# Kernel tuning notes

Hardware: AMD Instinct MI355X
Metric: run time of the kernel (lower is better)

The kernel has to match this reference:

```python
import jax, jax.numpy as jnp
import numpy as np

N_NODES = 100_000
N_EDGES = 1_600_000
N_FEAT = 128
N_HID = 64
N_CLASS = 10
N_LAYERS = 3
N_GRAPHS = 1000


def _linear_init(key, fan_in, fan_out):
    kw, kb = jax.random.split(key)
    s = 1.0 / np.sqrt(fan_in)
    w = jax.random.uniform(kw, (fan_in, fan_out), minval=-s, maxval=s, dtype=jnp.float32)
    b = jax.random.uniform(kb, (fan_out,), minval=-s, maxval=s, dtype=jnp.float32)
    return w, b


def setup_inputs() -> dict:
    key = jax.random.key(0)
    ks = jax.random.split(key, 16)
    x = jax.random.normal(ks[0], (N_NODES, N_FEAT), dtype=jnp.float32)
    edge_index = jax.random.randint(ks[1], (2, N_EDGES), 0, N_NODES, dtype=jnp.int64)
    batch = jnp.sort(jax.random.randint(ks[2], (N_NODES,), 0, N_GRAPHS, dtype=jnp.int64))

    pre_w, pre_b = _linear_init(ks[3], N_FEAT, N_HID)
    w1s, b1s, w2s, b2s = [], [], [], []
    for l in range(N_LAYERS):
        w1, b1 = _linear_init(jax.random.fold_in(ks[4], 2 * l), N_HID, N_HID)
        w2, b2 = _linear_init(jax.random.fold_in(ks[4], 2 * l + 1), N_HID, N_HID)
        w1s.append(w1); b1s.append(b1); w2s.append(w2); b2s.append(b2)
    post_w, post_b = _linear_init(ks[5], N_HID, N_HID)
    ro_w, ro_b = _linear_init(ks[6], N_HID, N_CLASS)

    return {
        "x": x, "edge_index": edge_index, "batch": batch,
        "pre_w": pre_w, "pre_b": pre_b,
        "conv_w1": jnp.stack(w1s), "conv_b1": jnp.stack(b1s),
        "conv_w2": jnp.stack(w2s), "conv_b2": jnp.stack(b2s),
        "post_w": post_w, "post_b": post_b,
        "ro_w": ro_w, "ro_b": ro_b,
    }


def reference(x, edge_index, batch, pre_w, pre_b, conv_w1, conv_b1, conv_w2, conv_b2, post_w, post_b, ro_w, ro_b):
    src = edge_index[0]  # message source (x_j)
    dst = edge_index[1]  # message target

    h = x @ pre_w + pre_b  # [N, H]
    for l in range(N_LAYERS):
        # GINConv, eps=0: MLP((1+eps)*h_i + sum_{j in N(i)} h_j)
        agg = jax.ops.segment_sum(h[src], dst, num_segments=N_NODES)
        z = h + agg
        z = jax.nn.relu(z @ conv_w1[l] + conv_b1[l]) @ conv_w2[l] + conv_b2[l]
        h = jax.nn.relu(z)  # dropout is identity in eval mode

    g = jax.ops.segment_sum(h, batch, num_segments=N_GRAPHS)  # global_add_pool [G, H]
    g = jax.nn.relu(g @ post_w + post_b)
    logits = g @ ro_w + ro_b
    return jax.nn.log_softmax(logits, axis=1)
```

## Files before the change

kernel.cpp:

```cpp
#include <hip/hip_runtime.h>
#include <math.h>

#define N_NODES  100000
#define N_FEAT   128
#define N_HID    64
#define N_CLASS  10
#define N_GRAPHS 1000
#define N_EDGES  1600000
#define NTILES   1563
#define BLK_N    128
#define NT2      782
#define HF_GROUPS 8
#define HF_RANGE 12500
#define HF_BLOCKS 2048
#define CSR_STRIDE 64
#define EMAX_LDS 32

typedef int iv4 __attribute__((ext_vector_type(4)));

__device__ __forceinline__ float bflo(unsigned u) { return __uint_as_float(u << 16); }
__device__ __forceinline__ float bfhi(unsigned u) { return __uint_as_float(u & 0xffff0000u); }
__device__ __forceinline__ unsigned bf_rne(float f) {
    unsigned u = __float_as_uint(f);
    return (u + 0x7fffu + ((u >> 16) & 1u)) >> 16;
}
__device__ __forceinline__ unsigned pack2(float a, float b) {
    return bf_rne(a) | (bf_rne(b) << 16);
}

__global__ __launch_bounds__(256, 4) void pre_kernel(
    const float* __restrict__ x, const float* __restrict__ W,
    const float* __restrict__ b, uint2* __restrict__ h)
{
    __shared__ float xs[64][68];
    __shared__ float ws[64][68];
    const int tid = threadIdx.x;
    const int tx = tid & 15, ty = tid >> 4;
    const int n0 = blockIdx.x * 64;

    float acc[4][4];
#pragma unroll
    for (int i = 0; i < 4; ++i)
#pragma unroll
        for (int j = 0; j < 4; ++j) acc[i][j] = 0.f;

    for (int p = 0; p < 2; ++p) {
        __syncthreads();
#pragma unroll
        for (int t = 0; t < 4; ++t) {
            const int idx = t * 256 + tid;
            const int m = idx >> 4, kv = idx & 15;
            float4 v = make_float4(0.f, 0.f, 0.f, 0.f);
            if (n0 + m < N_NODES)
                v = *(const float4*)(x + (size_t)(n0 + m) * N_FEAT + p * 64 + kv * 4);
            *(float4*)&xs[m][kv * 4] = v;
            *(float4*)&ws[m][kv * 4] =
                *(const float4*)(W + (size_t)(p * 64 + m) * N_HID + kv * 4);
        }
        __syncthreads();
#pragma unroll 2
        for (int k4 = 0; k4 < 16; ++k4) {
            float4 a[4], bb[4];
#pragma unroll
            for (int i = 0; i < 4; ++i)
                a[i] = *(const float4*)&xs[ty + 16 * i][k4 * 4];
#pragma unroll
            for (int j = 0; j < 4; ++j)
                bb[j] = *(const float4*)&ws[k4 * 4 + j][tx * 4];
#pragma unroll
            for (int i = 0; i < 4; ++i) {
                const float* ap = (const float*)&a[i];
#pragma unroll
                for (int j = 0; j < 4; ++j) {
                    const float* bp = (const float*)&bb[j];
#pragma unroll
                    for (int c = 0; c < 4; ++c)
                        acc[i][c] = fmaf(ap[j], bp[c], acc[i][c]);
                }
            }
        }
    }

    const float4 bias = *(const float4*)(b + tx * 4);
#pragma unroll
    for (int i = 0; i < 4; ++i) {
        const int node = n0 + ty + 16 * i;
        if (node < N_NODES) {
            h[(size_t)node * 16 + tx] = make_uint2(
                pack2(acc[i][0] + bias.x, acc[i][1] + bias.y),
                pack2(acc[i][2] + bias.z, acc[i][3] + bias.w));
        }
    }
}

__global__ __launch_bounds__(256) void hist_fill_kernel(
    const int* __restrict__ ei, int* __restrict__ deg, int* __restrict__ csr)
{
    const int r   = blockIdx.x & (HF_GROUPS - 1);
    const int g   = blockIdx.x >> 3;
    const int lo  = r * HF_RANGE;
    const int hi  = lo + HF_RANGE;
    const int gsz = (gridDim.x >> 3) * blockDim.x;
    const int t0  = g * blockDim.x + threadIdx.x;
    const iv4* dst4 = (const iv4*)(ei + N_EDGES);
    for (int q = t0; q < N_EDGES / 4; q += gsz) {
        const iv4 d = __builtin_nontemporal_load(dst4 + q);
        const int e0 = q * 4;
        if (d.x >= lo && d.x < hi) {
            int p = atomicAdd(&deg[d.x], 1);
            if (p < CSR_STRIDE)
                csr[d.x * CSR_STRIDE + p] = __builtin_nontemporal_load(ei + e0);
        }
        if (d.y >= lo && d.y < hi) {
            int p = atomicAdd(&deg[d.y], 1);
            if (p < CSR_STRIDE)
                csr[d.y * CSR_STRIDE + p] = __builtin_nontemporal_load(ei + e0 + 1);
        }
        if (d.z >= lo && d.z < hi) {
            int p = atomicAdd(&deg[d.z], 1);
            if (p < CSR_STRIDE)
                csr[d.z * CSR_STRIDE + p] = __builtin_nontemporal_load(ei + e0 + 2);
        }
        if (d.w >= lo && d.w < hi) {
            int p = atomicAdd(&deg[d.w], 1);
            if (p < CSR_STRIDE)
                csr[d.w * CSR_STRIDE + p] = __builtin_nontemporal_load(ei + e0 + 3);
        }
    }
}

__global__ __launch_bounds__(512, 6) void gather_mlp_kernel(
    const uint2* __restrict__ hin, uint2* __restrict__ hout,
    const int* __restrict__ csr, const int* __restrict__ deg,
    const float* __restrict__ W1, const float* __restrict__ b1,
    const float* __restrict__ W2, const float* __restrict__ b2)
{
    __shared__ float as[BLK_N][68];
    __shared__ float ws[64][68];
    __shared__ int   sdeg[BLK_N];
    const int tid = threadIdx.x;
    const int tx = tid & 15, ty = tid >> 4;
    const int sub = tx;
    const int n0 = blockIdx.x * BLK_N;

#pragma unroll
    for (int t = 0; t < 2; ++t) {
        const int idx = t * 512 + tid;
        const int m = idx >> 4, kv = idx & 15;
        *(float4*)&ws[m][kv * 4] = *(const float4*)(W1 + (size_t)m * N_HID + kv * 4);
    }
    if (tid < BLK_N) {
        const int node = n0 + tid;
        sdeg[tid] = (node < N_NODES) ? deg[node] : 0;
    }
#pragma unroll
    for (int t = 0; t < 2; ++t) {
        const int idx = t * 512 + tid;
        const int r = idx >> 3, s4 = idx & 7;
        const int node = n0 + r;
        int4 v = make_int4(0, 0, 0, 0);
        if (node < N_NODES)
            v = *(const int4*)(csr + (size_t)node * CSR_STRIDE + s4 * 4);
        *(int4*)((int*)&as[r][36] + s4 * 4) = v;
    }
    __syncthreads();

    for (int pp = 0; pp < 2; ++pp) {
        const int rA = ty + 64 * pp;
        const int rB = rA + 32;
        const int nodeA = n0 + rA;
        const int nodeB = n0 + rB;
        float aAx = 0.f, aAy = 0.f, aAz = 0.f, aAw = 0.f;
        float bAx = 0.f, bAy = 0.f, bAz = 0.f, bAw = 0.f;
        float aBx = 0.f, aBy = 0.f, aBz = 0.f, aBw = 0.f;
        float bBx = 0.f, bBy = 0.f, bBz = 0.f, bBw = 0.f;
        int nA = 0, nB = 0;
        if (nodeA < N_NODES) {
            nA = sdeg[rA]; nA = nA > CSR_STRIDE ? CSR_STRIDE : nA;
            const uint2 s = hin[(size_t)nodeA * 16 + sub];
            aAx = bflo(s.x); aAy = bfhi(s.x); aAz = bflo(s.y); aAw = bfhi(s.y);
        }
        if (nodeB < N_NODES) {
            nB = sdeg[rB]; nB = nB > CSR_STRIDE ? CSR_STRIDE : nB;
            const uint2 s = hin[(size_t)nodeB * 16 + sub];
            aBx = bflo(s.x); aBy = bfhi(s.x); aBz = bflo(s.y); aBw = bfhi(s.y);
        }
        const int nnA = nA > EMAX_LDS ? EMAX_LDS : nA;
        const int nnB = nB > EMAX_LDS ? EMAX_LDS : nB;
        const int* epA = (const int*)&as[rA][36];
        const int* epB = (const int*)&as[rB][36];
        const int mx = nnA > nnB ? nnA : nnB;
        for (int eb = 0; eb < mx; eb += 8) {
            uint2 rvA[8], rvB[8];
            const bool doA = eb < nnA;
            const bool doB = eb < nnB;
            if (doA) {
#pragma unroll
                for (int u = 0; u < 8; ++u) {
                    const int idx = eb + u;
                    const int cl = idx < nnA ? idx : nnA - 1;
                    rvA[u] = hin[(size_t)epA[cl] * 16 + sub];
                }
            }
            if (doB) {
#pragma unroll
                for (int u = 0; u < 8; ++u) {
                    const int idx = eb + u;
                    const int cl = idx < nnB ? idx : nnB - 1;
                    rvB[u] = hin[(size_t)epB[cl] * 16 + sub];
                }
            }
            if (doA) {
#pragma unroll
                for (int u = 0; u < 8; u += 2) {
                    if (eb + u < nnA) {
                        aAx += bflo(rvA[u].x); aAy += bfhi(rvA[u].x);
                        aAz += bflo(rvA[u].y); aAw += bfhi(rvA[u].y);
                    }
                    if (eb + u + 1 < nnA) {
                        bAx += bflo(rvA[u + 1].x); bAy += bfhi(rvA[u + 1].x);
                        bAz += bflo(rvA[u + 1].y); bAw += bfhi(rvA[u + 1].y);
                    }
                }
            }
            if (doB) {
#pragma unroll
                for (int u = 0; u < 8; u += 2) {
                    if (eb + u < nnB) {
                        aBx += bflo(rvB[u].x); aBy += bfhi(rvB[u].x);
                        aBz += bflo(rvB[u].y); aBw += bfhi(rvB[u].y);
                    }
                    if (eb + u + 1 < nnB) {
                        bBx += bflo(rvB[u + 1].x); bBy += bfhi(rvB[u + 1].x);
                        bBz += bflo(rvB[u + 1].y); bBw += bfhi(rvB[u + 1].y);
                    }
                }
            }
        }
        for (int t = EMAX_LDS; t < nA; ++t) {
            const int s0 = csr[(size_t)nodeA * CSR_STRIDE + t];
            const uint2 a = hin[(size_t)s0 * 16 + sub];
            aAx += bflo(a.x); aAy += bfhi(a.x);
            aAz += bflo(a.y); aAw += bfhi(a.y);
        }
        for (int t = EMAX_LDS; t < nB; ++t) {
            const int s0 = csr[(size_t)nodeB * CSR_STRIDE + t];
            const uint2 a = hin[(size_t)s0 * 16 + sub];
            aBx += bflo(a.x); aBy += bfhi(a.x);
            aBz += bflo(a.y); aBw += bfhi(a.y);
        }
        *(float4*)&as[rA][sub * 4] =
            make_float4(aAx + bAx, aAy + bAy, aAz + bAz, aAw + bAw);
        *(float4*)&as[rB][sub * 4] =
            make_float4(aBx + bBx, aBy + bBy, aBz + bBz, aBw + bBw);
    }
    __syncthreads();

    float acc[4][4];
#pragma unroll
    for (int i = 0; i < 4; ++i)
#pragma unroll
        for (int j = 0; j < 4; ++j) acc[i][j] = 0.f;
#pragma unroll 2
    for (int k4 = 0; k4 < 16; ++k4) {
        float4 a[4], bb[4];
#pragma unroll
        for (int i = 0; i < 4; ++i)
            a[i] = *(const float4*)&as[ty + 32 * i][k4 * 4];
#pragma unroll
        for (int j = 0; j < 4; ++j)
            bb[j] = *(const float4*)&ws[k4 * 4 + j][tx * 4];
#pragma unroll
        for (int i = 0; i < 4; ++i) {
            const float* ap = (const float*)&a[i];
#pragma unroll
            for (int j = 0; j < 4; ++j) {
                const float* bp = (const float*)&bb[j];
#pragma unroll
                for (int c = 0; c < 4; ++c)
                    acc[i][c] = fmaf(ap[j], bp[c], acc[i][c]);
            }
        }
    }
    const float4 bias1 = *(const float4*)(b1 + tx * 4);
    float4 z[4];
#pragma unroll
    for (int i = 0; i < 4; ++i) {
        z[i].x = fmaxf(acc[i][0] + bias1.x, 0.f);
        z[i].y = fmaxf(acc[i][1] + bias1.y, 0.f);
        z[i].z = fmaxf(acc[i][2] + bias1.z, 0.f);
        z[i].w = fmaxf(acc[i][3] + bias1.w, 0.f);
    }
    __syncthreads();
#pragma unroll
    for (int i = 0; i < 4; ++i)
        *(float4*)&as[ty + 32 * i][tx * 4] = z[i];
#pragma unroll
    for (int t = 0; t < 2; ++t) {
        const int idx = t * 512 + tid;
        const int m = idx >> 4, kv = idx & 15;
        *(float4*)&ws[m][kv * 4] = *(const float4*)(W2 + (size_t)m * N_HID + kv * 4);
    }
    __syncthreads();

#pragma unroll
    for (int i = 0; i < 4; ++i)
#pragma unroll
        for (int j = 0; j < 4; ++j) acc[i][j] = 0.f;
#pragma unroll 2
    for (int k4 = 0; k4 < 16; ++k4) {
        float4 a[4], bb[4];
#pragma unroll
        for (int i = 0; i < 4; ++i)
            a[i] = *(const float4*)&as[ty + 32 * i][k4 * 4];
#pragma unroll
        for (int j = 0; j < 4; ++j)
            bb[j] = *(const float4*)&ws[k4 * 4 + j][tx * 4];
#pragma unroll
        for (int i = 0; i < 4; ++i) {
            const float* ap = (const float*)&a[i];
#pragma unroll
            for (int j = 0; j < 4; ++j) {
                const float* bp = (const float*)&bb[j];
#pragma unroll
                for (int c = 0; c < 4; ++c)
                    acc[i][c] = fmaf(ap[j], bp[c], acc[i][c]);
            }
        }
    }
    const float4 bias2 = *(const float4*)(b2 + tx * 4);
#pragma unroll
    for (int i = 0; i < 4; ++i) {
        const int node = n0 + ty + 32 * i;
        if (node < N_NODES) {
            hout[(size_t)node * 16 + tx] = make_uint2(
                pack2(fmaxf(acc[i][0] + bias2.x, 0.f),
                      fmaxf(acc[i][1] + bias2.y, 0.f)),
                pack2(fmaxf(acc[i][2] + bias2.z, 0.f),
                      fmaxf(acc[i][3] + bias2.w, 0.f)));
        }
    }
}

__global__ __launch_bounds__(256) void pool_head_kernel(
    const unsigned short* __restrict__ h, const int* __restrict__ batch,
    const float* __restrict__ Wp, const float* __restrict__ bp,
    const float* __restrict__ Wr, const float* __restrict__ br,
    float* __restrict__ out)
{
    const int graph = blockIdx.x;
    int l = 0, r = N_NODES;
    while (l < r) { int m = (l + r) >> 1; if (batch[m] < graph) l = m + 1; else r = m; }
    const int lo = l;
    r = N_NODES;
    while (l < r) { int m = (l + r) >> 1; if (batch[m] < graph + 1) l = m + 1; else r = m; }
    const int hi = l;

    const int lane = threadIdx.x & 63;
    const int wave = threadIdx.x >> 6;
    float acc = 0.0f;
    for (int i = lo + wave; i < hi; i += 4)
        acc += __uint_as_float(((unsigned)h[(size_t)i * N_HID + lane]) << 16);
    __shared__ float sacc[4][N_HID];
    sacc[wave][lane] = acc;
    __syncthreads();
    if (wave != 0) return;

    const float gv = sacc[0][lane] + sacc[1][lane] + sacc[2][lane] + sacc[3][lane];
    float acc2 = bp[lane];
#pragma unroll
    for (int k = 0; k < N_HID; ++k) {
        const float gk = __int_as_float(
            __builtin_amdgcn_readlane(__float_as_int(gv), k));
        acc2 = fmaf(gk, Wp[k * N_HID + lane], acc2);
    }
    const float y = fmaxf(acc2, 0.f);

    float logit = (lane < N_CLASS) ? br[lane] : 0.f;
#pragma unroll
    for (int k = 0; k < N_HID; ++k) {
        const float yk = __int_as_float(
            __builtin_amdgcn_readlane(__float_as_int(y), k));
        if (lane < N_CLASS)
            logit = fmaf(yk, Wr[k * N_CLASS + lane], logit);
    }

    __shared__ float slog[N_CLASS];
    if (lane < N_CLASS) slog[lane] = logit;
    if (lane < N_CLASS) {
        float m = -INFINITY;
#pragma unroll
        for (int c = 0; c < N_CLASS; ++c) m = fmaxf(m, slog[c]);
        float sum = 0.0f;
#pragma unroll
        for (int c = 0; c < N_CLASS; ++c) sum += expf(slog[c] - m);
        out[(size_t)graph * N_CLASS + lane] = logit - m - logf(sum);
    }
}

extern "C" void kernel_launch(void* const* d_in, const int* in_sizes, int n_in,
                              void* d_out, int out_size, void* d_ws, size_t ws_size,
                              hipStream_t stream)
{
    const float* x       = (const float*)d_in[0];
    const int*   ei      = (const int*)d_in[1];
    const int*   batch   = (const int*)d_in[2];
    const float* pre_w   = (const float*)d_in[3];
    const float* pre_b   = (const float*)d_in[4];
    const float* conv_w1 = (const float*)d_in[5];
    const float* conv_b1 = (const float*)d_in[6];
    const float* conv_w2 = (const float*)d_in[7];
    const float* conv_b2 = (const float*)d_in[8];
    const float* post_w  = (const float*)d_in[9];
    const float* post_b  = (const float*)d_in[10];
    const float* ro_w    = (const float*)d_in[11];
    const float* ro_b    = (const float*)d_in[12];
    float* out = (float*)d_out;

    uint2* h0   = (uint2*)d_ws;
    uint2* h1   = h0 + (size_t)N_NODES * 16;
    int*   deg  = (int*)(h1 + (size_t)N_NODES * 16);
    int*   csr  = deg + N_NODES;

    (void)hipMemsetAsync(deg, 0, N_NODES * sizeof(int), stream);

    pre_kernel<<<NTILES, 256, 0, stream>>>(x, pre_w, pre_b, h0);
    hist_fill_kernel<<<HF_BLOCKS, 256, 0, stream>>>(ei, deg, csr);

    gather_mlp_kernel<<<NT2, 512, 0, stream>>>(
        h0, h1, csr, deg,
        conv_w1, conv_b1, conv_w2, conv_b2);
    gather_mlp_kernel<<<NT2, 512, 0, stream>>>(
        h1, h0, csr, deg,
        conv_w1 + N_HID * N_HID, conv_b1 + N_HID,
        conv_w2 + N_HID * N_HID, conv_b2 + N_HID);
    gather_mlp_kernel<<<NT2, 512, 0, stream>>>(
        h0, h1, csr, deg,
        conv_w1 + 2 * N_HID * N_HID, conv_b1 + 2 * N_HID,
        conv_w2 + 2 * N_HID * N_HID, conv_b2 + 2 * N_HID);

    pool_head_kernel<<<N_GRAPHS, 256, 0, stream>>>(
        (const unsigned short*)h1, batch, post_w, post_b, ro_w, ro_b, out);
}
```

Measured before the change: 402.3 us.

## Split fused gather+MLP kernel into separate gather and in-place MLP kernels

Each GIN layer's fused gather+MLP kernel is split in two. A smaller-block gather kernel (64 nodes, 256 threads) writes the aggregated features as bf16 to a global buffer, and an MLP kernel reads that buffer back and overwrites it in place. The aim is to raise occupancy and latency hiding for the gather, which is bound by irregular memory access, by removing the large LDS footprint of the GEMM stage. The cost is an extra bf16 round trip of the aggregate through global memory, extra kernel launches, and an added bf16 rounding of the aggregate sum before the MLP.

```diff
diff --git a/kernel.cpp b/kernel.cpp
--- a/kernel.cpp
+++ b/kernel.cpp
@@ -129,45 +129,36 @@
     }
 }
 
-__global__ __launch_bounds__(512, 6) void gather_mlp_kernel(
-    const uint2* __restrict__ hin, uint2* __restrict__ hout,
-    const int* __restrict__ csr, const int* __restrict__ deg,
-    const float* __restrict__ W1, const float* __restrict__ b1,
-    const float* __restrict__ W2, const float* __restrict__ b2)
-{
-    __shared__ float as[BLK_N][68];
-    __shared__ float ws[64][68];
-    __shared__ int   sdeg[BLK_N];
+__global__ __launch_bounds__(256, 6) void gather_kernel(
+    const uint2* __restrict__ hin, uint2* __restrict__ aggb,
+    const int* __restrict__ csr, const int* __restrict__ deg)
+{
+    __shared__ int es[64][32];
+    __shared__ int sdeg[64];
     const int tid = threadIdx.x;
     const int tx = tid & 15, ty = tid >> 4;
     const int sub = tx;
-    const int n0 = blockIdx.x * BLK_N;
-
-#pragma unroll
-    for (int t = 0; t < 2; ++t) {
-        const int idx = t * 512 + tid;
-        const int m = idx >> 4, kv = idx & 15;
-        *(float4*)&ws[m][kv * 4] = *(const float4*)(W1 + (size_t)m * N_HID + kv * 4);
-    }
-    if (tid < BLK_N) {
+    const int n0 = blockIdx.x * 64;
+
+    if (tid < 64) {
         const int node = n0 + tid;
         sdeg[tid] = (node < N_NODES) ? deg[node] : 0;
     }
 #pragma unroll
     for (int t = 0; t < 2; ++t) {
-        const int idx = t * 512 + tid;
+        const int idx = t * 256 + tid;
         const int r = idx >> 3, s4 = idx & 7;
         const int node = n0 + r;
         int4 v = make_int4(0, 0, 0, 0);
         if (node < N_NODES)
             v = *(const int4*)(csr + (size_t)node * CSR_STRIDE + s4 * 4);
-        *(int4*)((int*)&as[r][36] + s4 * 4) = v;
+        *(int4*)&es[r][s4 * 4] = v;
     }
     __syncthreads();
 
     for (int pp = 0; pp < 2; ++pp) {
-        const int rA = ty + 64 * pp;
-        const int rB = rA + 32;
+        const int rA = ty + 32 * pp;
+        const int rB = rA + 16;
         const int nodeA = n0 + rA;
         const int nodeB = n0 + rB;
         float aAx = 0.f, aAy = 0.f, aAz = 0.f, aAw = 0.f;
@@ -187,8 +178,8 @@
         }
         const int nnA = nA > EMAX_LDS ? EMAX_LDS : nA;
         const int nnB = nB > EMAX_LDS ? EMAX_LDS : nB;
-        const int* epA = (const int*)&as[rA][36];
-        const int* epB = (const int*)&as[rB][36];
+        const int* epA = &es[rA][0];
+        const int* epB = &es[rB][0];
         const int mx = nnA > nnB ? nnA : nnB;
         for (int eb = 0; eb < mx; eb += 8) {
             uint2 rvA[8], rvB[8];
@@ -249,10 +240,40 @@
             aBx += bflo(a.x); aBy += bfhi(a.x);
             aBz += bflo(a.y); aBw += bfhi(a.y);
         }
-        *(float4*)&as[rA][sub * 4] =
-            make_float4(aAx + bAx, aAy + bAy, aAz + bAz, aAw + bAw);
-        *(float4*)&as[rB][sub * 4] =
-            make_float4(aBx + bBx, aBy + bBy, aBz + bBz, aBw + bBw);
+        if (nodeA < N_NODES)
+            aggb[(size_t)nodeA * 16 + sub] = make_uint2(
+                pack2(aAx + bAx, aAy + bAy), pack2(aAz + bAz, aAw + bAw));
+        if (nodeB < N_NODES)
+            aggb[(size_t)nodeB * 16 + sub] = make_uint2(
+                pack2(aBx + bBx, aBy + bBy), pack2(aBz + bBz, aBw + bBw));
+    }
+}
+
+__global__ __launch_bounds__(512, 6) void mlp_kernel(
+    uint2* __restrict__ hbuf,
+    const float* __restrict__ W1, const float* __restrict__ b1,
+    const float* __restrict__ W2, const float* __restrict__ b2)
+{
+    __shared__ float as[BLK_N][68];
+    __shared__ float ws[64][68];
+    const int tid = threadIdx.x;
+    const int tx = tid & 15, ty = tid >> 4;
+    const int n0 = blockIdx.x * BLK_N;
+
+#pragma unroll
+    for (int t = 0; t < 2; ++t) {
+        const int idx = t * 512 + tid;
+        const int m = idx >> 4, kv = idx & 15;
+        *(float4*)&ws[m][kv * 4] = *(const float4*)(W1 + (size_t)m * N_HID + kv * 4);
+    }
+#pragma unroll
+    for (int t = 0; t < 4; ++t) {
+        const int idx = t * 512 + tid;
+        const int m = idx >> 4, kv = idx & 15;
+        uint2 v = make_uint2(0, 0);
+        if (n0 + m < N_NODES) v = hbuf[(size_t)(n0 + m) * 16 + kv];
+        as[m][kv * 4 + 0] = bflo(v.x); as[m][kv * 4 + 1] = bfhi(v.x);
+        as[m][kv * 4 + 2] = bflo(v.y); as[m][kv * 4 + 3] = bfhi(v.y);
     }
     __syncthreads();
 
@@ -333,7 +354,7 @@
     for (int i = 0; i < 4; ++i) {
         const int node = n0 + ty + 32 * i;
         if (node < N_NODES) {
-            hout[(size_t)node * 16 + tx] = make_uint2(
+            hbuf[(size_t)node * 16 + tx] = make_uint2(
                 pack2(fmaxf(acc[i][0] + bias2.x, 0.f),
                       fmaxf(acc[i][1] + bias2.y, 0.f)),
                 pack2(fmaxf(acc[i][2] + bias2.z, 0.f),
@@ -427,15 +448,16 @@
     pre_kernel<<<NTILES, 256, 0, stream>>>(x, pre_w, pre_b, h0);
     hist_fill_kernel<<<HF_BLOCKS, 256, 0, stream>>>(ei, deg, csr);
 
-    gather_mlp_kernel<<<NT2, 512, 0, stream>>>(
-        h0, h1, csr, deg,
-        conv_w1, conv_b1, conv_w2, conv_b2);
-    gather_mlp_kernel<<<NT2, 512, 0, stream>>>(
-        h1, h0, csr, deg,
+    gather_kernel<<<NTILES, 256, 0, stream>>>(h0, h1, csr, deg);
+    mlp_kernel<<<NT2, 512, 0, stream>>>(h1, conv_w1, conv_b1, conv_w2, conv_b2);
+
+    gather_kernel<<<NTILES, 256, 0, stream>>>(h1, h0, csr, deg);
+    mlp_kernel<<<NT2, 512, 0, stream>>>(h0,
         conv_w1 + N_HID * N_HID, conv_b1 + N_HID,
         conv_w2 + N_HID * N_HID, conv_b2 + N_HID);
-    gather_mlp_kernel<<<NT2, 512, 0, stream>>>(
-        h0, h1, csr, deg,
+
+    gather_kernel<<<NTILES, 256, 0, stream>>>(h0, h1, csr, deg);
+    mlp_kernel<<<NT2, 512, 0, stream>>>(h1,
         conv_w1 + 2 * N_HID * N_HID, conv_b1 + 2 * N_HID,
         conv_w2 + 2 * N_HID * N_HID, conv_b2 + 2 * N_HID);
 
```

Measured after the change: 419.5 us. +4.3%, slower.

## Use bf16 MFMA for GIN MLP with bf16 LDS tiles

Applied to the files above, without the earlier changes.

Replaces the scalar fp32 FMA GEMMs in the gather+MLP kernel with bf16 MFMA 16x16x32 instructions. Aggregated features, intermediate activations and the transposed W1/W2 weights are kept as bf16 in LDS, which also shrinks shared-memory use and may allow more resident blocks. The output is staged through LDS for a coalesced store. The cost is extra rounding of aggregated sums and hidden activations to bf16, plus a strided scalar weight transpose on load.

```diff
diff --git a/kernel.cpp b/kernel.cpp
--- a/kernel.cpp
+++ b/kernel.cpp
@@ -15,8 +15,11 @@
 #define HF_BLOCKS 2048
 #define CSR_STRIDE 64
 #define EMAX_LDS 32
+#define APITCH 72
 
 typedef int iv4 __attribute__((ext_vector_type(4)));
+typedef __attribute__((ext_vector_type(8))) __bf16 bf16x8;
+typedef __attribute__((ext_vector_type(4))) float f32x4;
 
 __device__ __forceinline__ float bflo(unsigned u) { return __uint_as_float(u << 16); }
 __device__ __forceinline__ float bfhi(unsigned u) { return __uint_as_float(u & 0xffff0000u); }
@@ -135,19 +138,18 @@
     const float* __restrict__ W1, const float* __restrict__ b1,
     const float* __restrict__ W2, const float* __restrict__ b2)
 {
-    __shared__ float as[BLK_N][68];
-    __shared__ float ws[64][68];
-    __shared__ int   sdeg[BLK_N];
+    __shared__ unsigned short asb[BLK_N][APITCH];
+    __shared__ unsigned short wsb[N_HID][APITCH];
+    __shared__ int sdeg[BLK_N];
     const int tid = threadIdx.x;
     const int tx = tid & 15, ty = tid >> 4;
     const int sub = tx;
     const int n0 = blockIdx.x * BLK_N;
 
 #pragma unroll
-    for (int t = 0; t < 2; ++t) {
+    for (int t = 0; t < 8; ++t) {
         const int idx = t * 512 + tid;
-        const int m = idx >> 4, kv = idx & 15;
-        *(float4*)&ws[m][kv * 4] = *(const float4*)(W1 + (size_t)m * N_HID + kv * 4);
+        wsb[idx & 63][idx >> 6] = (unsigned short)bf_rne(W1[idx]);
     }
     if (tid < BLK_N) {
         const int node = n0 + tid;
@@ -161,7 +163,7 @@
         int4 v = make_int4(0, 0, 0, 0);
         if (node < N_NODES)
             v = *(const int4*)(csr + (size_t)node * CSR_STRIDE + s4 * 4);
-        *(int4*)((int*)&as[r][36] + s4 * 4) = v;
+        *(int4*)((char*)&asb[r][0] + s4 * 16) = v;
     }
     __syncthreads();
 
@@ -187,8 +189,8 @@
         }
         const int nnA = nA > EMAX_LDS ? EMAX_LDS : nA;
         const int nnB = nB > EMAX_LDS ? EMAX_LDS : nB;
-        const int* epA = (const int*)&as[rA][36];
-        const int* epB = (const int*)&as[rB][36];
+        const int* epA = (const int*)&asb[rA][0];
+        const int* epB = (const int*)&asb[rB][0];
         const int mx = nnA > nnB ? nnA : nnB;
         for (int eb = 0; eb < mx; eb += 8) {
             uint2 rvA[8], rvB[8];
@@ -249,96 +251,83 @@
             aBx += bflo(a.x); aBy += bfhi(a.x);
             aBz += bflo(a.y); aBw += bfhi(a.y);
         }
-        *(float4*)&as[rA][sub * 4] =
-            make_float4(aAx + bAx, aAy + bAy, aAz + bAz, aAw + bAw);
-        *(float4*)&as[rB][sub * 4] =
-            make_float4(aBx + bBx, aBy + bBy, aBz + bBz, aBw + bBw);
-    }
-    __syncthreads();
-
-    float acc[4][4];
-#pragma unroll
-    for (int i = 0; i < 4; ++i)
-#pragma unroll
-        for (int j = 0; j < 4; ++j) acc[i][j] = 0.f;
-#pragma unroll 2
-    for (int k4 = 0; k4 < 16; ++k4) {
-        float4 a[4], bb[4];
-#pragma unroll
-        for (int i = 0; i < 4; ++i)
-            a[i] = *(const float4*)&as[ty + 32 * i][k4 * 4];
-#pragma unroll
-        for (int j = 0; j < 4; ++j)
-            bb[j] = *(const float4*)&ws[k4 * 4 + j][tx * 4];
-#pragma unroll
-        for (int i = 0; i < 4; ++i) {
-            const float* ap = (const float*)&a[i];
-#pragma unroll
-            for (int j = 0; j < 4; ++j) {
-                const float* bp = (const float*)&bb[j];
-#pragma unroll
-                for (int c = 0; c < 4; ++c)
-                    acc[i][c] = fmaf(ap[j], bp[c], acc[i][c]);
-            }
-        }
-    }
-    const float4 bias1 = *(const float4*)(b1 + tx * 4);
-    float4 z[4];
-#pragma unroll
-    for (int i = 0; i < 4; ++i) {
-        z[i].x = fmaxf(acc[i][0] + bias1.x, 0.f);
-        z[i].y = fmaxf(acc[i][1] + bias1.y, 0.f);
-        z[i].z = fmaxf(acc[i][2] + bias1.z, 0.f);
-        z[i].w = fmaxf(acc[i][3] + bias1.w, 0.f);
-    }
-    __syncthreads();
-#pragma unroll
-    for (int i = 0; i < 4; ++i)
-        *(float4*)&as[ty + 32 * i][tx * 4] = z[i];
-#pragma unroll
-    for (int t = 0; t < 2; ++t) {
+        *(uint2*)((char*)&asb[rA][0] + sub * 8) = make_uint2(
+            pack2(aAx + bAx, aAy + bAy), pack2(aAz + bAz, aAw + bAw));
+        *(uint2*)((char*)&asb[rB][0] + sub * 8) = make_uint2(
+            pack2(aBx + bBx, aBy + bBy), pack2(aBz + bBz, aBw + bBw));
+    }
+    __syncthreads();
+
+    const int wave = tid >> 6;
+    const int lane = tid & 63;
+    const int lr = lane & 15;
+    const int lg = lane >> 4;
+    const f32x4 vzero = {0.f, 0.f, 0.f, 0.f};
+
+    f32x4 acc[4] = {vzero, vzero, vzero, vzero};
+    {
+        const char* ar = (const char*)&asb[wave * 16 + lr][0] + lg * 16;
+        const bf16x8 a0 = *(const bf16x8*)ar;
+        const bf16x8 a1 = *(const bf16x8*)(ar + 64);
+#pragma unroll
+        for (int cb = 0; cb < 4; ++cb) {
+            const char* br = (const char*)&wsb[cb * 16 + lr][0] + lg * 16;
+            const bf16x8 w0 = *(const bf16x8*)br;
+            const bf16x8 w1 = *(const bf16x8*)(br + 64);
+            acc[cb] = __builtin_amdgcn_mfma_f32_16x16x32_bf16(a0, w0, acc[cb], 0, 0, 0);
+            acc[cb] = __builtin_amdgcn_mfma_f32_16x16x32_bf16(a1, w1, acc[cb], 0, 0, 0);
+        }
+    }
+#pragma unroll
+    for (int cb = 0; cb < 4; ++cb) {
+        const float bias = b1[cb * 16 + lr];
+#pragma unroll
+        for (int rg = 0; rg < 4; ++rg) {
+            const float v = fmaxf(acc[cb][rg] + bias, 0.f);
+            asb[wave * 16 + lg * 4 + rg][cb * 16 + lr] = (unsigned short)bf_rne(v);
+        }
+    }
+    __syncthreads();
+#pragma unroll
+    for (int t = 0; t < 8; ++t) {
+        const int idx = t * 512 + tid;
+        wsb[idx & 63][idx >> 6] = (unsigned short)bf_rne(W2[idx]);
+    }
+    __syncthreads();
+
+#pragma unroll
+    for (int cb = 0; cb < 4; ++cb) acc[cb] = vzero;
+    {
+        const char* ar = (const char*)&asb[wave * 16 + lr][0] + lg * 16;
+        const bf16x8 a0 = *(const bf16x8*)ar;
+        const bf16x8 a1 = *(const bf16x8*)(ar + 64);
+#pragma unroll
+        for (int cb = 0; cb < 4; ++cb) {
+            const char* br = (const char*)&wsb[cb * 16 + lr][0] + lg * 16;
+            const bf16x8 w0 = *(const bf16x8*)br;
+            const bf16x8 w1 = *(const bf16x8*)(br + 64);
+            acc[cb] = __builtin_amdgcn_mfma_f32_16x16x32_bf16(a0, w0, acc[cb], 0, 0, 0);
+            acc[cb] = __builtin_amdgcn_mfma_f32_16x16x32_bf16(a1, w1, acc[cb], 0, 0, 0);
+        }
+    }
+#pragma unroll
+    for (int cb = 0; cb < 4; ++cb) {
+        const float bias = b2[cb * 16 + lr];
+#pragma unroll
+        for (int rg = 0; rg < 4; ++rg) {
+            const float v = fmaxf(acc[cb][rg] + bias, 0.f);
+            asb[wave * 16 + lg * 4 + rg][cb * 16 + lr] = (unsigned short)bf_rne(v);
+        }
+    }
+    __syncthreads();
+
+#pragma unroll
+    for (int t = 0; t < 4; ++t) {
         const int idx = t * 512 + tid;
         const int m = idx >> 4, kv = idx & 15;
-        *(float4*)&ws[m][kv * 4] = *(const float4*)(W2 + (size_t)m * N_HID + kv * 4);
-    }
-    __syncthreads();
-
-#pragma unroll
-    for (int i = 0; i < 4; ++i)
-#pragma unroll
-        for (int j = 0; j < 4; ++j) acc[i][j] = 0.f;
-#pragma unroll 2
-    for (int k4 = 0; k4 < 16; ++k4) {
-        float4 a[4], bb[4];
-#pragma unroll
-        for (int i = 0; i < 4; ++i)
-            a[i] = *(const float4*)&as[ty + 32 * i][k4 * 4];
-#pragma unroll
-        for (int j = 0; j < 4; ++j)
-            bb[j] = *(const float4*)&ws[k4 * 4 + j][tx * 4];
-#pragma unroll
-        for (int i = 0; i < 4; ++i) {
-            const float* ap = (const float*)&a[i];
-#pragma unroll
-            for (int j = 0; j < 4; ++j) {
-                const float* bp = (const float*)&bb[j];
-#pragma unroll
-                for (int c = 0; c < 4; ++c)
-                    acc[i][c] = fmaf(ap[j], bp[c], acc[i][c]);
-            }
-        }
-    }
-    const float4 bias2 = *(const float4*)(b2 + tx * 4);
-#pragma unroll
-    for (int i = 0; i < 4; ++i) {
-        const int node = n0 + ty + 32 * i;
-        if (node < N_NODES) {
-            hout[(size_t)node * 16 + tx] = make_uint2(
-                pack2(fmaxf(acc[i][0] + bias2.x, 0.f),
-                      fmaxf(acc[i][1] + bias2.y, 0.f)),
-                pack2(fmaxf(acc[i][2] + bias2.z, 0.f),
-                      fmaxf(acc[i][3] + bias2.w, 0.f)));
-        }
+        if (n0 + m < N_NODES)
+            hout[(size_t)(n0 + m) * 16 + kv] =
+                *(const uint2*)((const char*)&asb[m][0] + kv * 8);
     }
 }
 
```

Result: faster. 379.1 us (-5.8%).
